# Optimization experiments

Measured on AMD Instinct MI355X. Metric: run time of the kernel, lower is better.

The kernel has to match this reference:

```python
import jax, jax.numpy as jnp
import numpy as np

EPS = 1e-5

def setup_inputs() -> dict:
    key = jax.random.key(0)
    ks = jax.random.split(key, 8)
    B, Cin, H, W = 16, 64, 512, 64
    Cout = 128  # out_channels == mid_channels (default) == NL1D channels
    return {
        "x": jax.random.normal(ks[0], (B, Cin, H, W), dtype=jnp.float32),
        "conv_w": jax.random.normal(ks[1], (Cout, Cin, 3, 3), dtype=jnp.float32) * 0.05,
        "bn1_g": jnp.ones((Cout,), jnp.float32),
        "bn1_b": jnp.zeros((Cout,), jnp.float32),
        "g_w": jax.random.normal(ks[2], (Cout, Cout), dtype=jnp.float32) * 0.05,
        "g_b": jnp.zeros((Cout,), jnp.float32),
        "out_w": jax.random.normal(ks[3], (Cout, Cout), dtype=jnp.float32) * 0.05,
        "out_b": jnp.zeros((Cout,), jnp.float32),
        "bn2_g": jnp.ones((Cout,), jnp.float32),
        "bn2_b": jnp.zeros((Cout,), jnp.float32),
    }

def _bn_train(x, gamma, beta):
    # BatchNorm2d in training mode: batch stats over (B, H, W) per channel
    mu = jnp.mean(x, axis=(0, 2, 3), keepdims=True)
    var = jnp.mean(jnp.square(x - mu), axis=(0, 2, 3), keepdims=True)
    xn = (x - mu) * jax.lax.rsqrt(var + EPS)
    return xn * gamma[None, :, None, None] + beta[None, :, None, None]

def reference(x, conv_w, bn1_g, bn1_b, g_w, g_b, out_w, out_b, bn2_g, bn2_b):
    # conv: 3x3, reflect padding, no bias -> BN -> ReLU
    xp = jnp.pad(x, ((0, 0), (0, 0), (1, 1), (1, 1)), mode="reflect")
    h = jax.lax.conv_general_dilated(
        xp, conv_w, window_strides=(1, 1), padding="VALID",
        dimension_numbers=("NCHW", "OIHW", "NCHW"))
    h = jax.nn.relu(_bn_train(h, bn1_g, bn1_b))  # [B, C, H, W]

    # NL1D
    B, C, Hh, W = h.shape
    xm = jnp.mean(h, axis=3)  # [B, C, H]
    # layer_norm over (C, H) per batch element, no affine
    mu = jnp.mean(xm, axis=(1, 2), keepdims=True)
    var = jnp.mean(jnp.square(xm - mu), axis=(1, 2), keepdims=True)
    xn = (xm - mu) * jax.lax.rsqrt(var + EPS)

    f = jnp.einsum("bch,bck->bhk", xn, xn) / jnp.sqrt(jnp.float32(C))
    f = jax.nn.softmax(f, axis=2)  # [B, H, H]

    y = jnp.einsum("mc,bch->bmh", g_w, xn) + g_b[None, :, None]  # conv1d 1x1
    y = jnp.einsum("bhk,bmk->bmh", f, y)  # bmm(f, y^T)^T
    y = jnp.einsum("om,bmh->boh", out_w, y) + out_b[None, :, None]  # [B, C, H]

    out = h + y[:, :, :, None]  # broadcast == repeat over W
    return jax.nn.silu(_bn_train(out, bn2_g, bn2_b))
```

## Files before the change

### kernel.cpp

```cpp
#include <hip/hip_runtime.h>
#include <stdint.h>

typedef __attribute__((ext_vector_type(8))) short short8;
typedef __attribute__((ext_vector_type(4))) float f32x4;

typedef const __attribute__((address_space(1))) unsigned int* gas_u32p;
typedef __attribute__((address_space(3))) unsigned int* las_u32p;

__device__ __forceinline__ unsigned short f2bf(float f){
  union{float f; unsigned u;} v; v.f = f;
  unsigned r = v.u + 0x7FFFu + ((v.u >> 16) & 1u);
  return (unsigned short)(r >> 16);
}
__device__ __forceinline__ void dec8(uint4 d, float* r){
  union{unsigned a; float f;} t;
  t.a = (d.x & 0xFFFFu) << 16; r[0]=t.f; t.a = d.x & 0xFFFF0000u; r[1]=t.f;
  t.a = (d.y & 0xFFFFu) << 16; r[2]=t.f; t.a = d.y & 0xFFFF0000u; r[3]=t.f;
  t.a = (d.z & 0xFFFFu) << 16; r[4]=t.f; t.a = d.z & 0xFFFF0000u; r[5]=t.f;
  t.a = (d.w & 0xFFFFu) << 16; r[6]=t.f; t.a = d.w & 0xFFFF0000u; r[7]=t.f;
}

__global__ __launch_bounds__(256) void k_prep(const float* __restrict__ cw,
                                              unsigned short* __restrict__ wA){
  int i = blockIdx.x*256 + threadIdx.x;
  if(i >= 18*128*32) return;
  int kk = i & 31, m = (i >> 5) & 127, ks = i >> 12;
  int k = ks*32 + kk;
  int pos = k >> 6, cin = k & 63;
  int dh = pos/3, dw = pos - dh*3;
  wA[i] = f2bf(cw[((m*64 + cin)*3 + dh)*3 + dw]);
}

__global__ __launch_bounds__(256) void k_xbf(const float* __restrict__ x,
                                             unsigned short* __restrict__ xbf){
  const int h = blockIdx.x, b = blockIdx.y;
  __shared__ float L[64][65];
  const int t = threadIdx.x;
  #pragma unroll
  for(int i=0;i<4;++i){
    int idx = i*256 + t;
    int c = idx >> 4, w0 = (idx & 15) * 4;
    const float* p = x + (((size_t)b*64 + c)*512 + h)*64 + w0;
    float4 v = *(const float4*)p;
    L[c][w0] = v.x; L[c][w0+1] = v.y; L[c][w0+2] = v.z; L[c][w0+3] = v.w;
  }
  __syncthreads();
  unsigned short* dst = xbf + (((size_t)b*512 + h) << 12);
  #pragma unroll
  for(int i=0;i<8;++i){
    int idx = i*256 + t;
    int w = idx >> 5, c2 = (idx & 31)*2;
    unsigned pk = (unsigned)f2bf(L[c2][w]) | ((unsigned)f2bf(L[c2+1][w]) << 16);
    *(unsigned*)(dst + (w<<6) + c2) = pk;
  }
}

__global__ __launch_bounds__(256, 2) void k_conv(
    const unsigned short* __restrict__ xbf, const unsigned short* __restrict__ wA,
    unsigned short* __restrict__ craw, float* __restrict__ sum_slots,
    float* __restrict__ sq_slots)
{
  const int b = blockIdx.y;
  const int bx = blockIdx.x;
  const int hx = (bx & 7)*16 + (bx >> 3);
  const int h0 = hx * 4;
  __shared__ __align__(16) unsigned short xs[6*4096];
  __shared__ float red[2][128];
  const int t = threadIdx.x;
  const int lane = t & 63, wv = t >> 6;
  for(int r = wv; r < 6; r += 4){
    int hin = h0 - 1 + r;
    hin = hin < 0 ? 1 : (hin > 511 ? 510 : hin);
    const unsigned short* rsrc = xbf + (((size_t)b*512 + hin) << 12);
    unsigned short* ldsrow = &xs[r*4096];
    #pragma unroll
    for(int it=0; it<8; ++it){
      int o = it*1024 + lane*16;
      int w = o >> 7;
      int q = o & 127;
      int so = (w << 7) + (q ^ (((w >> 1) & 7) << 4));
      __builtin_amdgcn_global_load_lds(
          (gas_u32p)(const void*)((const char*)rsrc + so),
          (las_u32p)(void*)(ldsrow + it*512), 16, 0, 0);
    }
  }
  const int r15 = lane & 15, quad = lane >> 4;
  int P[4][3];
  #pragma unroll
  for(int nt=0;nt<4;++nt){
    int wn = (nt>>1)*32 + 2*r15 + (nt&1);
    #pragma unroll
    for(int dw=0;dw<3;++dw){
      int wi = wn + dw - 1;
      wi = wi < 0 ? 1 : (wi > 63 ? 62 : wi);
      int s = ((wi >> 1) & 7) << 4;
      P[nt][dw] = (wi << 7) + ((quad*16) ^ (s & 0x30)) + (s & 0x40);
    }
  }
  f32x4 acc[8][4];
  #pragma unroll
  for(int mt=0;mt<8;++mt)
    #pragma unroll
    for(int nt=0;nt<4;++nt){ f32x4 z = {0.f,0.f,0.f,0.f}; acc[mt][nt] = z; }
  const unsigned short* wbase = wA + r15*32 + quad*8;
  __syncthreads();
  const char* xsb = (const char*)xs;
  #pragma unroll
  for(int ks=0; ks<18; ++ks){
    const int pos = ks >> 1;
    const int dh = pos/3, dw = pos - dh*3;
    const int kbit = (ks & 1) << 6;
    const int rowoff = (wv + dh)*8192;
    short8 a[8];
    const unsigned short* wk = wbase + ks*4096;
    #pragma unroll
    for(int mt=0;mt<8;++mt) a[mt] = *(const short8*)(wk + mt*512);
    short8 bfr[4];
    #pragma unroll
    for(int nt=0;nt<4;++nt)
      bfr[nt] = *(const short8*)(xsb + rowoff + (P[nt][dw] ^ kbit));
    #pragma unroll
    for(int mt=0;mt<8;++mt){
      #pragma unroll
      for(int nt=0;nt<4;++nt)
        acc[mt][nt] = __builtin_amdgcn_mfma_f32_16x16x32_bf16(a[mt], bfr[nt], acc[mt][nt], 0,0,0);
    }
  }
  {
    size_t obase = (((size_t)b*128)*512 + (size_t)(h0+wv))*64 + 2*r15;
    #pragma unroll
    for(int mt=0;mt<8;++mt){
      #pragma unroll
      for(int rg=0;rg<4;++rg){
        int co = mt*16 + quad*4 + rg;
        unsigned pk0 = (unsigned)f2bf(acc[mt][0][rg]) | ((unsigned)f2bf(acc[mt][1][rg]) << 16);
        unsigned pk1 = (unsigned)f2bf(acc[mt][2][rg]) | ((unsigned)f2bf(acc[mt][3][rg]) << 16);
        __builtin_nontemporal_store(pk0, (unsigned*)(craw + obase + (size_t)co*32768));
        __builtin_nontemporal_store(pk1, (unsigned*)(craw + obase + (size_t)co*32768 + 32));
      }
    }
  }
  if(t < 128){ red[0][t] = 0.f; red[1][t] = 0.f; }
  __syncthreads();
  #pragma unroll
  for(int mt=0;mt<8;++mt){
    #pragma unroll
    for(int rg=0;rg<4;++rg){
      float s = acc[mt][0][rg] + acc[mt][1][rg] + acc[mt][2][rg] + acc[mt][3][rg];
      float q = acc[mt][0][rg]*acc[mt][0][rg] + acc[mt][1][rg]*acc[mt][1][rg]
              + acc[mt][2][rg]*acc[mt][2][rg] + acc[mt][3][rg]*acc[mt][3][rg];
      #pragma unroll
      for(int m=1;m<16;m<<=1){ s += __shfl_xor(s, m); q += __shfl_xor(q, m); }
      if(r15 == 0){
        int co = mt*16 + quad*4 + rg;
        atomicAdd(&red[0][co], s);
        atomicAdd(&red[1][co], q);
      }
    }
  }
  __syncthreads();
  if(t < 128){
    int slot = bx & 63;
    atomicAdd(&sum_slots[t*64 + slot], red[0][t]);
    atomicAdd(&sq_slots[t*64 + slot], red[1][t]);
  }
}

__global__ __launch_bounds__(256) void k_bn1fin(
    const float* __restrict__ sum_slots, const float* __restrict__ sq_slots,
    const float* __restrict__ g1, const float* __restrict__ b1,
    float* __restrict__ s1, float* __restrict__ t1)
{
  int c = threadIdx.x; if(c >= 128) return;
  double S = 0.0, Q = 0.0;
  for(int s=0;s<64;++s){ S += (double)sum_slots[c*64+s]; Q += (double)sq_slots[c*64+s]; }
  const double N = 524288.0;
  double mu = S/N, var = Q/N - mu*mu;
  float sc = (float)((double)g1[c] / sqrt(var + 1e-5));
  s1[c] = sc;
  t1[c] = (float)((double)b1[c] - mu*(double)sc);
}

__global__ __launch_bounds__(256) void k_passB(
    const unsigned short* __restrict__ craw, const float* __restrict__ s1,
    const float* __restrict__ t1, float* __restrict__ xm,
    float* __restrict__ Sh, float* __restrict__ Qh,
    float* __restrict__ lnS, float* __restrict__ lnQ)
{
  const int c = blockIdx.x, b = blockIdx.y;
  const int t = threadIdx.x, wv = t >> 6, l = t & 63;
  const float sc = s1[c], sf = t1[c];
  const unsigned short* base = craw + (((size_t)b*128 + c)*512)*64;
  float* xrow = xm + ((size_t)b*128 + c)*512;
  float sa = 0.f, qa = 0.f, la = 0.f;
  for(int it=0; it<16; ++it){
    int row = it*32 + wv*8 + (l >> 3);
    int w0 = (l & 7)*8;
    uint4 d = *(const uint4*)(base + (size_t)row*64 + w0);
    float r[8]; dec8(d, r);
    float tot = 0.f;
    #pragma unroll
    for(int j=0;j<8;++j){
      float v = sc*r[j] + sf;
      v = v > 0.f ? v : 0.f;
      tot += v; sa += v; qa += v*v;
    }
    tot += __shfl_xor(tot, 1); tot += __shfl_xor(tot, 2); tot += __shfl_xor(tot, 4);
    if((l & 7) == 0){
      float mv = tot * (1.f/64.f);
      xrow[row] = mv;
      la += mv*mv;
    }
  }
  #pragma unroll
  for(int m=1;m<64;m<<=1){
    sa += __shfl_xor(sa, m); qa += __shfl_xor(qa, m); la += __shfl_xor(la, m);
  }
  __shared__ float rs[4], rq[4], rl[4];
  if(l == 0){ rs[wv]=sa; rq[wv]=qa; rl[wv]=la; }
  __syncthreads();
  if(t == 0){
    float S = rs[0]+rs[1]+rs[2]+rs[3];
    float Q = rq[0]+rq[1]+rq[2]+rq[3];
    float L = rl[0]+rl[1]+rl[2]+rl[3];
    atomicAdd(&Sh[c], S);
    atomicAdd(&Qh[c], Q);
    atomicAdd(&lnS[b], S * (1.f/64.f));
    atomicAdd(&lnQ[b], L);
  }
}

__global__ __launch_bounds__(256) void k_lnfin(
    const float* __restrict__ lnS, const float* __restrict__ lnQ,
    float* __restrict__ ln_mu, float* __restrict__ ln_rs)
{
  int b = threadIdx.x; if(b >= 16) return;
  double mu = (double)lnS[b] / 65536.0;
  double var = (double)lnQ[b] / 65536.0 - mu*mu;
  ln_mu[b] = (float)mu;
  ln_rs[b] = (float)(1.0 / sqrt(var + 1e-5));
}

__global__ __launch_bounds__(256) void k_y1(
    const float* __restrict__ xm, const float* __restrict__ ln_mu,
    const float* __restrict__ ln_rs, const float* __restrict__ gw,
    const float* __restrict__ gb, float* __restrict__ y1)
{
  const int kt = blockIdx.x, b = blockIdx.y;
  __shared__ __align__(16) float GT[128*132];
  __shared__ __align__(16) float XN[128*68];
  const int t = threadIdx.x;
  const int k0 = kt*64;
  const float mu = ln_mu[b], rs = ln_rs[b];
  #pragma unroll
  for(int i=0;i<16;++i){
    int idx = t + i*256;
    int c4 = (idx & 31)*4, o = idx >> 5;
    float4 v = *(const float4*)&gw[o*128 + c4];
    GT[(c4+0)*132 + o] = v.x; GT[(c4+1)*132 + o] = v.y;
    GT[(c4+2)*132 + o] = v.z; GT[(c4+3)*132 + o] = v.w;
  }
  #pragma unroll
  for(int i=0;i<8;++i){
    int idx = t + i*256;
    int kk4 = (idx & 15)*4, c = idx >> 4;
    float4 v = *(const float4*)&xm[((size_t)b*128 + c)*512 + k0 + kk4];
    XN[c*68 + kk4 + 0] = (v.x - mu)*rs; XN[c*68 + kk4 + 1] = (v.y - mu)*rs;
    XN[c*68 + kk4 + 2] = (v.z - mu)*rs; XN[c*68 + kk4 + 3] = (v.w - mu)*rs;
  }
  __syncthreads();
  const int tx = t & 15, ty = t >> 4;
  float acc[8][4] = {{0}};
  for(int c=0;c<128;++c){
    f32x4 a0 = *(const f32x4*)&GT[c*132 + ty*8];
    f32x4 a1 = *(const f32x4*)&GT[c*132 + ty*8 + 4];
    f32x4 bv = *(const f32x4*)&XN[c*68 + tx*4];
    #pragma unroll
    for(int j=0;j<4;++j){
      #pragma unroll
      for(int i=0;i<4;++i){ acc[i][j] += a0[i]*bv[j]; acc[i+4][j] += a1[i]*bv[j]; }
    }
  }
  #pragma unroll
  for(int i=0;i<8;++i){
    int m = ty*8 + i;
    float bias = gb[m];
    f32x4 o;
    #pragma unroll
    for(int j=0;j<4;++j) o[j] = acc[i][j] + bias;
    *(f32x4*)&y1[((size_t)b*128 + m)*512 + k0 + tx*4] = o;
  }
}

__global__ __launch_bounds__(256) void k_att(
    const float* __restrict__ xm, const float* __restrict__ ln_mu,
    const float* __restrict__ ln_rs, const float* __restrict__ y1,
    const float* __restrict__ ow, const float* __restrict__ obv,
    float* __restrict__ y3,
    float* __restrict__ SyS, float* __restrict__ SyyS, float* __restrict__ SxyS)
{
  const int ht = blockIdx.x, b = blockIdx.y;
  const int h0 = ht*32;
  const int SP = 528;
  __shared__ __align__(16) float S[32*528];
  __shared__ __align__(16) float XH[128*32];
  __shared__ __align__(16) float BUF[8704];
  const int t = threadIdx.x;
  const int tx = t & 15, ty = t >> 4;
  const int lane = t & 63, wv = t >> 6;
  const float mu = ln_mu[b], rs = ln_rs[b];
  const float* xb = xm + (size_t)b*128*512;
  #pragma unroll
  for(int i=0;i<4;++i){
    int idx = t + i*256;
    int hh4 = (idx & 7)*4, c = idx >> 3;
    float4 v = *(const float4*)&xb[(size_t)c*512 + h0 + hh4];
    XH[c*32 + hh4 + 0] = (v.x - mu)*rs; XH[c*32 + hh4 + 1] = (v.y - mu)*rs;
    XH[c*32 + hh4 + 2] = (v.z - mu)*rs; XH[c*32 + hh4 + 3] = (v.w - mu)*rs;
  }
  const float sscale = 0.088388347648318447f;
  for(int kt=0;kt<8;++kt){
    int k0 = kt*64;
    #pragma unroll
    for(int i=0;i<8;++i){
      int idx = t + i*256;
      int kk4 = (idx & 15)*4, c = idx >> 4;
      float4 v = *(const float4*)&xb[(size_t)c*512 + k0 + kk4];
      BUF[c*68 + kk4 + 0] = (v.x - mu)*rs; BUF[c*68 + kk4 + 1] = (v.y - mu)*rs;
      BUF[c*68 + kk4 + 2] = (v.z - mu)*rs; BUF[c*68 + kk4 + 3] = (v.w - mu)*rs;
    }
    __syncthreads();
    float acc[2][4] = {{0}};
    for(int c=0;c<128;++c){
      float a0 = XH[c*32 + ty*2];
      float a1 = XH[c*32 + ty*2 + 1];
      f32x4 bv = *(const f32x4*)&BUF[c*68 + tx*4];
      #pragma unroll
      for(int j=0;j<4;++j){ acc[0][j] += a0*bv[j]; acc[1][j] += a1*bv[j]; }
    }
    #pragma unroll
    for(int i=0;i<2;++i){
      f32x4 o;
      #pragma unroll
      for(int j=0;j<4;++j) o[j] = acc[i][j]*sscale;
      *(f32x4*)&S[(ty*2+i)*SP + k0 + tx*4] = o;
    }
    __syncthreads();
  }
  #pragma unroll
  for(int rr=0;rr<8;++rr){
    int row = wv*8 + rr;
    float* rowp = &S[row*SP];
    f32x4 v0 = *(const f32x4*)&rowp[lane*8];
    f32x4 v1 = *(const f32x4*)&rowp[lane*8 + 4];
    float mx = v0[0];
    #pragma unroll
    for(int j=1;j<4;++j) mx = fmaxf(mx, v0[j]);
    #pragma unroll
    for(int j=0;j<4;++j) mx = fmaxf(mx, v1[j]);
    #pragma unroll
    for(int m=1;m<64;m<<=1) mx = fmaxf(mx, __shfl_xor(mx, m));
    float sum = 0.f;
    #pragma unroll
    for(int j=0;j<4;++j){ v0[j] = __expf(v0[j]-mx); sum += v0[j]; }
    #pragma unroll
    for(int j=0;j<4;++j){ v1[j] = __expf(v1[j]-mx); sum += v1[j]; }
    #pragma unroll
    for(int m=1;m<64;m<<=1) sum += __shfl_xor(sum, m);
    float inv = 1.f / sum;
    #pragma unroll
    for(int j=0;j<4;++j){ v0[j] *= inv; v1[j] *= inv; }
    *(f32x4*)&rowp[lane*8] = v0;
    *(f32x4*)&rowp[lane*8+4] = v1;
  }
  __syncthreads();
  float y2a[2][8] = {{0}};
  for(int kt=0;kt<8;++kt){
    int k0 = kt*64;
    #pragma unroll
    for(int i=0;i<8;++i){
      int idx = t + i*256;
      int kk4 = (idx & 15)*4, m = idx >> 4;
      float4 v = *(const float4*)&y1[((size_t)b*128 + m)*512 + k0 + kk4];
      BUF[(kk4+0)*132 + m] = v.x; BUF[(kk4+1)*132 + m] = v.y;
      BUF[(kk4+2)*132 + m] = v.z; BUF[(kk4+3)*132 + m] = v.w;
    }
    __syncthreads();
    for(int kk=0;kk<64;++kk){
      float a0 = S[(ty*2)*SP + k0 + kk];
      float a1 = S[(ty*2+1)*SP + k0 + kk];
      f32x4 b0 = *(const f32x4*)&BUF[kk*132 + tx*8];
      f32x4 b1 = *(const f32x4*)&BUF[kk*132 + tx*8 + 4];
      #pragma unroll
      for(int j=0;j<4;++j){
        y2a[0][j]   += a0*b0[j]; y2a[1][j]   += a1*b0[j];
        y2a[0][j+4] += a0*b1[j]; y2a[1][j+4] += a1*b1[j];
      }
    }
    __syncthreads();
  }
  #pragma unroll
  for(int i=0;i<2;++i)
    #pragma unroll
    for(int j=0;j<8;++j)
      BUF[(ty*2+i)*131 + tx*8 + j] = y2a[i][j];
  float* OWT = S;
  #pragma unroll
  for(int i=0;i<16;++i){
    int idx = t + i*256;
    int m4 = (idx & 31)*4, o = idx >> 5;
    float4 v = *(const float4*)&ow[o*128 + m4];
    OWT[(m4+0)*132 + o] = v.x; OWT[(m4+1)*132 + o] = v.y;
    OWT[(m4+2)*132 + o] = v.z; OWT[(m4+3)*132 + o] = v.w;
  }
  __syncthreads();
  float a2[2][8] = {{0}};
  for(int m=0;m<128;++m){
    f32x4 w0 = *(const f32x4*)&OWT[m*132 + ty*8];
    f32x4 w1 = *(const f32x4*)&OWT[m*132 + ty*8 + 4];
    float h0v = BUF[(tx*2)*131 + m];
    float h1v = BUF[(tx*2+1)*131 + m];
    #pragma unroll
    for(int j=0;j<4;++j){
      a2[0][j]   += w0[j]*h0v; a2[1][j]   += w0[j]*h1v;
      a2[0][j+4] += w1[j]*h0v; a2[1][j+4] += w1[j]*h1v;
    }
  }
  const int slot = ((ht<<4) | b) & 31;
  #pragma unroll
  for(int j=0;j<8;++j){
    int o = ty*8 + j;
    float bias = obv[o];
    float v0 = a2[0][j] + bias;
    float v1 = a2[1][j] + bias;
    size_t off = ((size_t)b*128 + o)*512 + h0 + tx*2;
    float2 st; st.x = v0; st.y = v1;
    *(float2*)&y3[off] = st;
    float2 xv = *(const float2*)&xm[off];
    float sy_ = v0 + v1;
    float syy_ = v0*v0 + v1*v1;
    float sxy_ = v0*xv.x + v1*xv.y;
    #pragma unroll
    for(int m=1;m<16;m<<=1){
      sy_ += __shfl_xor(sy_, m); syy_ += __shfl_xor(syy_, m); sxy_ += __shfl_xor(sxy_, m);
    }
    if(tx == 0){
      atomicAdd(&SyS[o*32 + slot], sy_);
      atomicAdd(&SyyS[o*32 + slot], syy_);
      atomicAdd(&SxyS[o*32 + slot], sxy_);
    }
  }
}

__global__ __launch_bounds__(256) void k_bn2fin(
    const float* __restrict__ Sh, const float* __restrict__ Qh,
    const float* __restrict__ SyS, const float* __restrict__ SyyS,
    const float* __restrict__ SxyS, const float* __restrict__ g2,
    const float* __restrict__ b2, float* __restrict__ s2, float* __restrict__ t2)
{
  int c = threadIdx.x; if(c >= 128) return;
  double Sy = 0.0, Syy = 0.0, Sxy = 0.0;
  for(int s=0;s<32;++s){
    Sy  += (double)SyS[c*32+s];
    Syy += (double)SyyS[c*32+s];
    Sxy += (double)SxyS[c*32+s];
  }
  const double N = 524288.0;
  double S2 = (double)Sh[c] + 64.0*Sy;
  double Q2 = (double)Qh[c] + 128.0*Sxy + 64.0*Syy;
  double mu = S2/N, var = Q2/N - mu*mu;
  float sc = (float)((double)g2[c] / sqrt(var + 1e-5));
  s2[c] = sc;
  t2[c] = (float)((double)b2[c] - mu*(double)sc);
}

__global__ __launch_bounds__(256) void k_final(
    const unsigned short* __restrict__ craw, const float* __restrict__ s1,
    const float* __restrict__ t1, const float* __restrict__ y3,
    const float* __restrict__ s2, const float* __restrict__ t2,
    float* __restrict__ out)
{
  const int c = blockIdx.x, b = blockIdx.y;
  const int t = threadIdx.x, wv = t >> 6, l = t & 63;
  const float a1 = s1[c], c1 = t1[c], a2 = s2[c], c2 = t2[c];
  const size_t rb = ((size_t)b*128 + c)*512;
  const unsigned short* base = craw + rb*64;
  const float* yrow = y3 + rb;
  float* ob = out + rb*64;
  for(int it=0; it<16; ++it){
    int row = it*32 + wv*8 + (l >> 3);
    int w0 = (l & 7)*8;
    uint4 d = *(const uint4*)(base + (size_t)row*64 + w0);
    float yv = yrow[row];
    float r[8]; dec8(d, r);
    f32x4 o0, o1;
    #pragma unroll
    for(int j=0;j<8;++j){
      float h = a1*r[j] + c1; h = h > 0.f ? h : 0.f;
      float z = a2*(h + yv) + c2;
      float val = z * __builtin_amdgcn_rcpf(1.f + __expf(-z));
      if(j < 4) o0[j] = val; else o1[j-4] = val;
    }
    *(f32x4*)(ob + (size_t)row*64 + w0) = o0;
    *(f32x4*)(ob + (size_t)row*64 + w0 + 4) = o1;
  }
}

extern "C" void kernel_launch(void* const* d_in, const int* in_sizes, int n_in,
                              void* d_out, int out_size, void* d_ws, size_t ws_size,
                              hipStream_t stream)
{
  const float* x      = (const float*)d_in[0];
  const float* conv_w = (const float*)d_in[1];
  const float* bn1_g  = (const float*)d_in[2];
  const float* bn1_b  = (const float*)d_in[3];
  const float* g_w    = (const float*)d_in[4];
  const float* g_b    = (const float*)d_in[5];
  const float* out_w  = (const float*)d_in[6];
  const float* out_b  = (const float*)d_in[7];
  const float* bn2_g  = (const float*)d_in[8];
  const float* bn2_b  = (const float*)d_in[9];
  float* out = (float*)d_out;
  char* ws = (char*)d_ws;

  float* sum_slots = (float*)(ws);
  float* sq_slots  = (float*)(ws + 32768);
  float* SyS       = (float*)(ws);
  float* SyyS      = (float*)(ws + 16384);
  float* SxyS      = (float*)(ws + 32768);
  float* Sh        = (float*)(ws + 65536);
  float* Qh        = (float*)(ws + 66048);
  float* lnS       = (float*)(ws + 66560);
  float* lnQ       = (float*)(ws + 66624);
  float* s1        = (float*)(ws + 66688);
  float* t1        = (float*)(ws + 67200);
  float* ln_mu     = (float*)(ws + 67712);
  float* ln_rs     = (float*)(ws + 67776);
  float* s2        = (float*)(ws + 67840);
  float* t2        = (float*)(ws + 68352);
  unsigned short* wA = (unsigned short*)(ws + 70400);
  float* y3        = (float*)(ws + 217856);
  unsigned short* craw = (unsigned short*)(ws + 4412160);

  float* xm  = out;
  float* y1  = out + 2*(1u<<20);
  unsigned short* xbf = (unsigned short*)((char*)out + (size_t)64*1024*1024);

  hipMemsetAsync(ws, 0, 66688, stream);
  hipLaunchKernelGGL(k_prep,   dim3(288),      dim3(256), 0, stream, conv_w, wA);
  hipLaunchKernelGGL(k_xbf,    dim3(512,16),   dim3(256), 0, stream, x, xbf);
  hipLaunchKernelGGL(k_conv,   dim3(128,16),   dim3(256), 0, stream, xbf, wA, craw, sum_slots, sq_slots);
  hipLaunchKernelGGL(k_bn1fin, dim3(1),        dim3(128), 0, stream, sum_slots, sq_slots, bn1_g, bn1_b, s1, t1);
  hipMemsetAsync(ws, 0, 49152, stream);
  hipLaunchKernelGGL(k_passB,  dim3(128,16),   dim3(256), 0, stream, craw, s1, t1, xm, Sh, Qh, lnS, lnQ);
  hipLaunchKernelGGL(k_lnfin,  dim3(1),        dim3(64),  0, stream, lnS, lnQ, ln_mu, ln_rs);
  hipLaunchKernelGGL(k_y1,     dim3(8,16),     dim3(256), 0, stream, xm, ln_mu, ln_rs, g_w, g_b, y1);
  hipLaunchKernelGGL(k_att,    dim3(16,16),    dim3(256), 0, stream, xm, ln_mu, ln_rs, y1, out_w, out_b, y3, SyS, SyyS, SxyS);
  hipLaunchKernelGGL(k_bn2fin, dim3(1),        dim3(128), 0, stream, Sh, Qh, SyS, SyyS, SxyS, bn2_g, bn2_b, s2, t2);
  hipLaunchKernelGGL(k_final,  dim3(128,16),   dim3(256), 0, stream, craw, s1, t1, y3, s2, t2, out);
}
```

Before: 739.9 us.

## Fold BN/LN finalize kernels into consumers, stage conv weights in LDS, nontemporal IO

Removes the three single-block finalize kernels (bn1fin, lnfin, bn2fin) and one memset by recomputing the per-channel and per-batch coefficients inside each consumer block. The workspace is re-laid out so every accumulator slot is cleared by one memset. In the conv kernel, weights are double-buffered into LDS with async global-to-LDS loads, the MFMA block gets a higher wave priority, and a barrier is added each k-step. Streaming loads and stores become nontemporal. The trade is redundant coefficient math in every block plus 18 extra barriers in the conv loop.

After: 694.2 us. 1.07x faster.

```diff
diff --git a/kernel.cpp b/kernel.cpp
--- a/kernel.cpp
+++ b/kernel.cpp
@@ -3,6 +3,7 @@
 
 typedef __attribute__((ext_vector_type(8))) short short8;
 typedef __attribute__((ext_vector_type(4))) float f32x4;
+typedef __attribute__((ext_vector_type(4))) unsigned int u32x4;
 
 typedef const __attribute__((address_space(1))) unsigned int* gas_u32p;
 typedef __attribute__((address_space(3))) unsigned int* las_u32p;
@@ -12,12 +13,12 @@
   unsigned r = v.u + 0x7FFFu + ((v.u >> 16) & 1u);
   return (unsigned short)(r >> 16);
 }
-__device__ __forceinline__ void dec8(uint4 d, float* r){
+__device__ __forceinline__ void dec8(u32x4 d, float* r){
   union{unsigned a; float f;} t;
-  t.a = (d.x & 0xFFFFu) << 16; r[0]=t.f; t.a = d.x & 0xFFFF0000u; r[1]=t.f;
-  t.a = (d.y & 0xFFFFu) << 16; r[2]=t.f; t.a = d.y & 0xFFFF0000u; r[3]=t.f;
-  t.a = (d.z & 0xFFFFu) << 16; r[4]=t.f; t.a = d.z & 0xFFFF0000u; r[5]=t.f;
-  t.a = (d.w & 0xFFFFu) << 16; r[6]=t.f; t.a = d.w & 0xFFFF0000u; r[7]=t.f;
+  t.a = (d[0] & 0xFFFFu) << 16; r[0]=t.f; t.a = d[0] & 0xFFFF0000u; r[1]=t.f;
+  t.a = (d[1] & 0xFFFFu) << 16; r[2]=t.f; t.a = d[1] & 0xFFFF0000u; r[3]=t.f;
+  t.a = (d[2] & 0xFFFFu) << 16; r[4]=t.f; t.a = d[2] & 0xFFFF0000u; r[5]=t.f;
+  t.a = (d[3] & 0xFFFFu) << 16; r[6]=t.f; t.a = d[3] & 0xFFFF0000u; r[7]=t.f;
 }
 
 __global__ __launch_bounds__(256) void k_prep(const float* __restrict__ cw,
@@ -41,8 +42,8 @@
     int idx = i*256 + t;
     int c = idx >> 4, w0 = (idx & 15) * 4;
     const float* p = x + (((size_t)b*64 + c)*512 + h)*64 + w0;
-    float4 v = *(const float4*)p;
-    L[c][w0] = v.x; L[c][w0+1] = v.y; L[c][w0+2] = v.z; L[c][w0+3] = v.w;
+    f32x4 v = __builtin_nontemporal_load((const f32x4*)p);
+    L[c][w0] = v[0]; L[c][w0+1] = v[1]; L[c][w0+2] = v[2]; L[c][w0+3] = v[3];
   }
   __syncthreads();
   unsigned short* dst = xbf + (((size_t)b*512 + h) << 12);
@@ -65,6 +66,7 @@
   const int hx = (bx & 7)*16 + (bx >> 3);
   const int h0 = hx * 4;
   __shared__ __align__(16) unsigned short xs[6*4096];
+  __shared__ __align__(16) unsigned short wbuf[2][4096];
   __shared__ float red[2][128];
   const int t = threadIdx.x;
   const int lane = t & 63, wv = t >> 6;
@@ -84,6 +86,13 @@
           (las_u32p)(void*)(ldsrow + it*512), 16, 0, 0);
     }
   }
+  #pragma unroll
+  for(int j=0;j<2;++j){
+    int off = j*2048 + wv*512;
+    __builtin_amdgcn_global_load_lds(
+        (gas_u32p)(const void*)(wA + off + lane*8),
+        (las_u32p)(void*)(&wbuf[0][off]), 16, 0, 0);
+  }
   const int r15 = lane & 15, quad = lane >> 4;
   int P[4][3];
   #pragma unroll
@@ -102,29 +111,43 @@
   for(int mt=0;mt<8;++mt)
     #pragma unroll
     for(int nt=0;nt<4;++nt){ f32x4 z = {0.f,0.f,0.f,0.f}; acc[mt][nt] = z; }
-  const unsigned short* wbase = wA + r15*32 + quad*8;
   __syncthreads();
   const char* xsb = (const char*)xs;
   #pragma unroll
   for(int ks=0; ks<18; ++ks){
+    if(ks < 17){
+      const unsigned short* wsrc = wA + (ks+1)*4096;
+      unsigned short* wdst = &wbuf[(ks+1)&1][0];
+      #pragma unroll
+      for(int j=0;j<2;++j){
+        int off = j*2048 + wv*512;
+        __builtin_amdgcn_global_load_lds(
+            (gas_u32p)(const void*)(wsrc + off + lane*8),
+            (las_u32p)(void*)(wdst + off), 16, 0, 0);
+      }
+    }
     const int pos = ks >> 1;
     const int dh = pos/3, dw = pos - dh*3;
     const int kbit = (ks & 1) << 6;
     const int rowoff = (wv + dh)*8192;
+    const unsigned short* wk = &wbuf[ks&1][0];
     short8 a[8];
-    const unsigned short* wk = wbase + ks*4096;
-    #pragma unroll
-    for(int mt=0;mt<8;++mt) a[mt] = *(const short8*)(wk + mt*512);
+    #pragma unroll
+    for(int mt=0;mt<8;++mt)
+      a[mt] = *(const short8*)(wk + mt*512 + r15*32 + quad*8);
     short8 bfr[4];
     #pragma unroll
     for(int nt=0;nt<4;++nt)
       bfr[nt] = *(const short8*)(xsb + rowoff + (P[nt][dw] ^ kbit));
+    __builtin_amdgcn_s_setprio(1);
     #pragma unroll
     for(int mt=0;mt<8;++mt){
       #pragma unroll
       for(int nt=0;nt<4;++nt)
         acc[mt][nt] = __builtin_amdgcn_mfma_f32_16x16x32_bf16(a[mt], bfr[nt], acc[mt][nt], 0,0,0);
     }
+    __builtin_amdgcn_s_setprio(0);
+    __syncthreads();
   }
   {
     size_t obase = (((size_t)b*128)*512 + (size_t)(h0+wv))*64 + 2*r15;
@@ -166,37 +189,39 @@
   }
 }
 
-__global__ __launch_bounds__(256) void k_bn1fin(
-    const float* __restrict__ sum_slots, const float* __restrict__ sq_slots,
-    const float* __restrict__ g1, const float* __restrict__ b1,
-    float* __restrict__ s1, float* __restrict__ t1)
-{
-  int c = threadIdx.x; if(c >= 128) return;
+__device__ __forceinline__ void bn1_coeff(
+    const float* sum_slots, const float* sq_slots,
+    const float* g1, const float* b1, int c, float* a1, float* c1)
+{
   double S = 0.0, Q = 0.0;
+  #pragma unroll
   for(int s=0;s<64;++s){ S += (double)sum_slots[c*64+s]; Q += (double)sq_slots[c*64+s]; }
   const double N = 524288.0;
   double mu = S/N, var = Q/N - mu*mu;
   float sc = (float)((double)g1[c] / sqrt(var + 1e-5));
-  s1[c] = sc;
-  t1[c] = (float)((double)b1[c] - mu*(double)sc);
+  *a1 = sc;
+  *c1 = (float)((double)b1[c] - mu*(double)sc);
 }
 
 __global__ __launch_bounds__(256) void k_passB(
-    const unsigned short* __restrict__ craw, const float* __restrict__ s1,
-    const float* __restrict__ t1, float* __restrict__ xm,
+    const unsigned short* __restrict__ craw,
+    const float* __restrict__ sum_slots, const float* __restrict__ sq_slots,
+    const float* __restrict__ g1, const float* __restrict__ b1,
+    float* __restrict__ xm,
     float* __restrict__ Sh, float* __restrict__ Qh,
     float* __restrict__ lnS, float* __restrict__ lnQ)
 {
   const int c = blockIdx.x, b = blockIdx.y;
   const int t = threadIdx.x, wv = t >> 6, l = t & 63;
-  const float sc = s1[c], sf = t1[c];
+  float sc, sf;
+  bn1_coeff(sum_slots, sq_slots, g1, b1, c, &sc, &sf);
   const unsigned short* base = craw + (((size_t)b*128 + c)*512)*64;
   float* xrow = xm + ((size_t)b*128 + c)*512;
   float sa = 0.f, qa = 0.f, la = 0.f;
   for(int it=0; it<16; ++it){
     int row = it*32 + wv*8 + (l >> 3);
     int w0 = (l & 7)*8;
-    uint4 d = *(const uint4*)(base + (size_t)row*64 + w0);
+    u32x4 d = __builtin_nontemporal_load((const u32x4*)(base + (size_t)row*64 + w0));
     float r[8]; dec8(d, r);
     float tot = 0.f;
     #pragma unroll
@@ -230,20 +255,18 @@
   }
 }
 
-__global__ __launch_bounds__(256) void k_lnfin(
-    const float* __restrict__ lnS, const float* __restrict__ lnQ,
-    float* __restrict__ ln_mu, float* __restrict__ ln_rs)
-{
-  int b = threadIdx.x; if(b >= 16) return;
+__device__ __forceinline__ void ln_coeff(const float* lnS, const float* lnQ,
+                                         int b, float* mu_o, float* rs_o)
+{
   double mu = (double)lnS[b] / 65536.0;
   double var = (double)lnQ[b] / 65536.0 - mu*mu;
-  ln_mu[b] = (float)mu;
-  ln_rs[b] = (float)(1.0 / sqrt(var + 1e-5));
+  *mu_o = (float)mu;
+  *rs_o = (float)(1.0 / sqrt(var + 1e-5));
 }
 
 __global__ __launch_bounds__(256) void k_y1(
-    const float* __restrict__ xm, const float* __restrict__ ln_mu,
-    const float* __restrict__ ln_rs, const float* __restrict__ gw,
+    const float* __restrict__ xm, const float* __restrict__ lnS,
+    const float* __restrict__ lnQ, const float* __restrict__ gw,
     const float* __restrict__ gb, float* __restrict__ y1)
 {
   const int kt = blockIdx.x, b = blockIdx.y;
@@ -251,7 +274,8 @@
   __shared__ __align__(16) float XN[128*68];
   const int t = threadIdx.x;
   const int k0 = kt*64;
-  const float mu = ln_mu[b], rs = ln_rs[b];
+  float mu, rs;
+  ln_coeff(lnS, lnQ, b, &mu, &rs);
   #pragma unroll
   for(int i=0;i<16;++i){
     int idx = t + i*256;
@@ -293,8 +317,8 @@
 }
 
 __global__ __launch_bounds__(256) void k_att(
-    const float* __restrict__ xm, const float* __restrict__ ln_mu,
-    const float* __restrict__ ln_rs, const float* __restrict__ y1,
+    const float* __restrict__ xm, const float* __restrict__ lnS,
+    const float* __restrict__ lnQ, const float* __restrict__ y1,
     const float* __restrict__ ow, const float* __restrict__ obv,
     float* __restrict__ y3,
     float* __restrict__ SyS, float* __restrict__ SyyS, float* __restrict__ SxyS)
@@ -308,7 +332,8 @@
   const int t = threadIdx.x;
   const int tx = t & 15, ty = t >> 4;
   const int lane = t & 63, wv = t >> 6;
-  const float mu = ln_mu[b], rs = ln_rs[b];
+  float mu, rs;
+  ln_coeff(lnS, lnQ, b, &mu, &rs);
   const float* xb = xm + (size_t)b*128*512;
   #pragma unroll
   for(int i=0;i<4;++i){
@@ -452,14 +477,22 @@
   }
 }
 
-__global__ __launch_bounds__(256) void k_bn2fin(
+__global__ __launch_bounds__(256) void k_final(
+    const unsigned short* __restrict__ craw,
+    const float* __restrict__ sum_slots, const float* __restrict__ sq_slots,
+    const float* __restrict__ g1, const float* __restrict__ b1,
     const float* __restrict__ Sh, const float* __restrict__ Qh,
     const float* __restrict__ SyS, const float* __restrict__ SyyS,
     const float* __restrict__ SxyS, const float* __restrict__ g2,
-    const float* __restrict__ b2, float* __restrict__ s2, float* __restrict__ t2)
-{
-  int c = threadIdx.x; if(c >= 128) return;
+    const float* __restrict__ b2, const float* __restrict__ y3,
+    float* __restrict__ out)
+{
+  const int c = blockIdx.x, b = blockIdx.y;
+  const int t = threadIdx.x, wv = t >> 6, l = t & 63;
+  float a1, c1;
+  bn1_coeff(sum_slots, sq_slots, g1, b1, c, &a1, &c1);
   double Sy = 0.0, Syy = 0.0, Sxy = 0.0;
+  #pragma unroll
   for(int s=0;s<32;++s){
     Sy  += (double)SyS[c*32+s];
     Syy += (double)SyyS[c*32+s];
@@ -468,21 +501,9 @@
   const double N = 524288.0;
   double S2 = (double)Sh[c] + 64.0*Sy;
   double Q2 = (double)Qh[c] + 128.0*Sxy + 64.0*Syy;
-  double mu = S2/N, var = Q2/N - mu*mu;
-  float sc = (float)((double)g2[c] / sqrt(var + 1e-5));
-  s2[c] = sc;
-  t2[c] = (float)((double)b2[c] - mu*(double)sc);
-}
-
-__global__ __launch_bounds__(256) void k_final(
-    const unsigned short* __restrict__ craw, const float* __restrict__ s1,
-    const float* __restrict__ t1, const float* __restrict__ y3,
-    const float* __restrict__ s2, const float* __restrict__ t2,
-    float* __restrict__ out)
-{
-  const int c = blockIdx.x, b = blockIdx.y;
-  const int t = threadIdx.x, wv = t >> 6, l = t & 63;
-  const float a1 = s1[c], c1 = t1[c], a2 = s2[c], c2 = t2[c];
+  double mu2 = S2/N, var2 = Q2/N - mu2*mu2;
+  const float a2 = (float)((double)g2[c] / sqrt(var2 + 1e-5));
+  const float c2 = (float)((double)b2[c] - mu2*(double)a2);
   const size_t rb = ((size_t)b*128 + c)*512;
   const unsigned short* base = craw + rb*64;
   const float* yrow = y3 + rb;
@@ -490,7 +511,7 @@
   for(int it=0; it<16; ++it){
     int row = it*32 + wv*8 + (l >> 3);
     int w0 = (l & 7)*8;
-    uint4 d = *(const uint4*)(base + (size_t)row*64 + w0);
+    u32x4 d = __builtin_nontemporal_load((const u32x4*)(base + (size_t)row*64 + w0));
     float yv = yrow[row];
     float r[8]; dec8(d, r);
     f32x4 o0, o1;
@@ -501,8 +522,8 @@
       float val = z * __builtin_amdgcn_rcpf(1.f + __expf(-z));
       if(j < 4) o0[j] = val; else o1[j-4] = val;
     }
-    *(f32x4*)(ob + (size_t)row*64 + w0) = o0;
-    *(f32x4*)(ob + (size_t)row*64 + w0 + 4) = o1;
+    __builtin_nontemporal_store(o0, (f32x4*)(ob + (size_t)row*64 + w0));
+    __builtin_nontemporal_store(o1, (f32x4*)(ob + (size_t)row*64 + w0 + 4));
   }
 }
 
@@ -525,37 +546,27 @@
 
   float* sum_slots = (float*)(ws);
   float* sq_slots  = (float*)(ws + 32768);
-  float* SyS       = (float*)(ws);
-  float* SyyS      = (float*)(ws + 16384);
-  float* SxyS      = (float*)(ws + 32768);
-  float* Sh        = (float*)(ws + 65536);
-  float* Qh        = (float*)(ws + 66048);
-  float* lnS       = (float*)(ws + 66560);
-  float* lnQ       = (float*)(ws + 66624);
-  float* s1        = (float*)(ws + 66688);
-  float* t1        = (float*)(ws + 67200);
-  float* ln_mu     = (float*)(ws + 67712);
-  float* ln_rs     = (float*)(ws + 67776);
-  float* s2        = (float*)(ws + 67840);
-  float* t2        = (float*)(ws + 68352);
-  unsigned short* wA = (unsigned short*)(ws + 70400);
-  float* y3        = (float*)(ws + 217856);
-  unsigned short* craw = (unsigned short*)(ws + 4412160);
+  float* SyS       = (float*)(ws + 65536);
+  float* SyyS      = (float*)(ws + 81920);
+  float* SxyS      = (float*)(ws + 98304);
+  float* Sh        = (float*)(ws + 114688);
+  float* Qh        = (float*)(ws + 115200);
+  float* lnS       = (float*)(ws + 115712);
+  float* lnQ       = (float*)(ws + 115776);
+  unsigned short* wA = (unsigned short*)(ws + 116224);
+  float* y3        = (float*)(ws + 263680);
+  unsigned short* craw = (unsigned short*)(ws + 4457984);
 
   float* xm  = out;
   float* y1  = out + 2*(1u<<20);
   unsigned short* xbf = (unsigned short*)((char*)out + (size_t)64*1024*1024);
 
-  hipMemsetAsync(ws, 0, 66688, stream);
+  hipMemsetAsync(ws, 0, 115840, stream);
   hipLaunchKernelGGL(k_prep,   dim3(288),      dim3(256), 0, stream, conv_w, wA);
   hipLaunchKernelGGL(k_xbf,    dim3(512,16),   dim3(256), 0, stream, x, xbf);
   hipLaunchKernelGGL(k_conv,   dim3(128,16),   dim3(256), 0, stream, xbf, wA, craw, sum_slots, sq_slots);
-  hipLaunchKernelGGL(k_bn1fin, dim3(1),        dim3(128), 0, stream, sum_slots, sq_slots, bn1_g, bn1_b, s1, t1);
-  hipMemsetAsync(ws, 0, 49152, stream);
-  hipLaunchKernelGGL(k_passB,  dim3(128,16),   dim3(256), 0, stream, craw, s1, t1, xm, Sh, Qh, lnS, lnQ);
-  hipLaunchKernelGGL(k_lnfin,  dim3(1),        dim3(64),  0, stream, lnS, lnQ, ln_mu, ln_rs);
-  hipLaunchKernelGGL(k_y1,     dim3(8,16),     dim3(256), 0, stream, xm, ln_mu, ln_rs, g_w, g_b, y1);
-  hipLaunchKernelGGL(k_att,    dim3(16,16),    dim3(256), 0, stream, xm, ln_mu, ln_rs, y1, out_w, out_b, y3, SyS, SyyS, SxyS);
-  hipLaunchKernelGGL(k_bn2fin, dim3(1),        dim3(128), 0, stream, Sh, Qh, SyS, SyyS, SxyS, bn2_g, bn2_b, s2, t2);
-  hipLaunchKernelGGL(k_final,  dim3(128,16),   dim3(256), 0, stream, craw, s1, t1, y3, s2, t2, out);
-}
+  hipLaunchKernelGGL(k_passB,  dim3(128,16),   dim3(256), 0, stream, craw, sum_slots, sq_slots, bn1_g, bn1_b, xm, Sh, Qh, lnS, lnQ);
+  hipLaunchKernelGGL(k_y1,     dim3(8,16),     dim3(256), 0, stream, xm, lnS, lnQ, g_w, g_b, y1);
+  hipLaunchKernelGGL(k_att,    dim3(16,16),    dim3(256), 0, stream, xm, lnS, lnQ, y1, out_w, out_b, y3, SyS, SyyS, SxyS);
+  hipLaunchKernelGGL(k_final,  dim3(128,16),   dim3(256), 0, stream, craw, sum_slots, sq_slots, bn1_g, bn1_b, Sh, Qh, SyS, SyyS, SxyS, bn2_g, bn2_b, y3, out);
+}
```
